# Optimization experiments

Measured on AMD Instinct MI355X. Metric: run time of the kernel, lower is better.

## Reference

```python
import jax, jax.numpy as jnp
import numpy as np

D_MODEL = 1024
EPS_DT = 1e-4
LN_EPS = 1e-5


def _layernorm(y, gamma, beta):
    mu = jnp.mean(y, axis=-1, keepdims=True)
    var = jnp.var(y, axis=-1, keepdims=True)
    return (y - mu) * jax.lax.rsqrt(var + LN_EPS) * gamma + beta


def setup_inputs() -> dict:
    key = jax.random.key(0)
    ks = jax.random.split(key, 8)
    B, T, D = 8, 4096, D_MODEL
    s = 1.0 / np.sqrt(D)  # ~ torch Linear default init scale
    return {
        "x": jax.random.normal(ks[0], (B, T, D), jnp.float32),
        "delta_t": jax.random.uniform(ks[1], (B, T, D), jnp.float32),
        "log_decay": jnp.zeros((D,), jnp.float32),
        "W_in": jax.random.uniform(ks[2], (D, D), jnp.float32, -s, s),
        "b_in": jax.random.uniform(ks[3], (D,), jnp.float32, -s, s),
        "W_gate": jax.random.uniform(ks[4], (D, D), jnp.float32, -s, s),
        "b_gate": jax.random.uniform(ks[5], (D,), jnp.float32, -s, s),
        "W_out": jax.random.uniform(ks[6], (D, D), jnp.float32, -s, s),
        "b_out": jax.random.uniform(ks[7], (D,), jnp.float32, -s, s),
        "gamma": jnp.ones((D,), jnp.float32),
        "beta": jnp.zeros((D,), jnp.float32),
    }


def reference(x, delta_t, log_decay, W_in, b_in, W_gate, b_gate, W_out, b_out, gamma, beta):
    B, T, D = x.shape
    decay = jax.nn.softplus(log_decay) + 1e-4          # [D]
    dt = jnp.maximum(delta_t, EPS_DT)                   # [B,T,D]
    lamb = jnp.exp(-decay * dt)                         # [B,T,D]
    # Drive terms depend only on x -> precompute in parallel (big GEMMs).
    update = jnp.einsum('btd,ed->bte', x, W_in) + b_in
    gate = jax.nn.sigmoid(jnp.einsum('btd,ed->bte', x, W_gate) + b_gate)
    drive = (1.0 - lamb) * gate * update                # [B,T,D]

    def step(state, inputs):
        l_t, d_t = inputs
        state = l_t * state + d_t
        return state, state

    state0 = jnp.zeros((B, D), x.dtype)
    final_state, states = jax.lax.scan(
        step, state0,
        (jnp.swapaxes(lamb, 0, 1), jnp.swapaxes(drive, 0, 1)))
    states = jnp.swapaxes(states, 0, 1)                 # [B,T,D]
    # dropout is identity in eval mode
    y = states + jnp.einsum('btd,ed->bte', states, W_out) + b_out
    out = _layernorm(y, gamma, beta)
    return out, final_state
```

## Files before the change

### kernel.cpp

```cpp
#include <hip/hip_runtime.h>
#include <hip/hip_bf16.h>

#define D_MODEL 1024
#define BATCH 8
#define SEQ 4096
#define MROWS (BATCH*SEQ)
#define NC 64
#define CL 64

typedef __attribute__((ext_vector_type(4))) float f32x4;
typedef __attribute__((ext_vector_type(8))) short s16x8;

__device__ __forceinline__ unsigned short f2bf(float f){
  union { float f; unsigned int u; } v; v.f = f;
  return (unsigned short)((v.u + 0x7fffu + ((v.u >> 16) & 1u)) >> 16);
}
__device__ __forceinline__ float bf2f(unsigned int bits){
  union { unsigned int u; float f; } v; v.u = bits << 16; return v.f;
}

__device__ __forceinline__ void gload16(const void* g, void* l){
  __builtin_amdgcn_global_load_lds(
      (const __attribute__((address_space(1))) unsigned int*)g,
      (__attribute__((address_space(3))) unsigned int*)l, 16, 0, 0);
}

__global__ __launch_bounds__(256)
void prep_all_kernel(const float* __restrict__ x,
                     const float* __restrict__ Wi, const float* __restrict__ Wg,
                     const float* __restrict__ Wo, const float* __restrict__ ld,
                     unsigned short* __restrict__ xb,
                     unsigned short* __restrict__ Wugb,
                     unsigned short* __restrict__ Wob,
                     float* __restrict__ decay, int nx4){
  const int b = blockIdx.x;
  if (b < 8192){
    int i = b*256 + threadIdx.x;
    for (; i < nx4; i += 8192*256){
      float4 v = ((const float4*)x)[i];
      ushort4 o;
      o.x = f2bf(v.x); o.y = f2bf(v.y); o.z = f2bf(v.z); o.w = f2bf(v.w);
      ((ushort4*)xb)[i] = o;
    }
  } else {
    const int i = (b-8192)*256 + threadIdx.x;
    float4 a = ((const float4*)Wi)[i]; ushort4 o;
    o.x=f2bf(a.x); o.y=f2bf(a.y); o.z=f2bf(a.z); o.w=f2bf(a.w); ((ushort4*)Wugb)[i]=o;
    a = ((const float4*)Wg)[i];
    o.x=f2bf(a.x); o.y=f2bf(a.y); o.z=f2bf(a.z); o.w=f2bf(a.w); ((ushort4*)Wugb)[i + D_MODEL*D_MODEL/4]=o;
    a = ((const float4*)Wo)[i];
    o.x=f2bf(a.x); o.y=f2bf(a.y); o.z=f2bf(a.z); o.w=f2bf(a.w); ((ushort4*)Wob)[i]=o;
    if (i < D_MODEL){
      float v = ld[i];
      float sp = fmaxf(v, 0.f) + log1pf(expf(-fabsf(v)));
      decay[i] = sp + 1e-4f;
    }
  }
}

__global__ __launch_bounds__(256, 3)
void gemm_ug_kernel(const unsigned short* __restrict__ Aglob,
                    const unsigned short* __restrict__ Bglob,
                    const float* __restrict__ b_in,
                    const float* __restrict__ b_gate,
                    unsigned short* __restrict__ ub,
                    unsigned short* __restrict__ gb)
{
  __shared__ unsigned short sA[128*64];
  __shared__ unsigned short sB[128*64];
  const int tid  = threadIdx.x;
  const int lane = tid & 63;
  const int wave = tid >> 6;
  const int wr = wave >> 1, wc = wave & 1;
  const int bid  = blockIdx.x;
  const int idx  = bid >> 3;
  const int xcd  = bid & 7;
  const int bcol = (idx & 15) * 128;
  const int brow = (xcd*32 + (idx >> 4)) * 128;

  const f32x4 zero = {0.f,0.f,0.f,0.f};
  f32x4 acc[4][4];
  #pragma unroll
  for (int a=0;a<4;a++)
    #pragma unroll
    for (int b=0;b<4;b++) acc[a][b]=zero;

  for (int kt = 0; kt < D_MODEL/64; ++kt){
    __syncthreads();
    #pragma unroll
    for (int i=0;i<4;i++){
      const int ob = i*256 + wave*64;
      const int o  = ob + lane;
      const int r  = o >> 3;
      const int c  = ((o & 7) ^ (r & 7)) * 16;
      gload16((const char*)Aglob + (size_t)(brow + r)*(D_MODEL*2) + (size_t)kt*128 + c,
              (char*)sA + (size_t)ob*16);
      gload16((const char*)Bglob + (size_t)(bcol + r)*(D_MODEL*2) + (size_t)kt*128 + c,
              (char*)sB + (size_t)ob*16);
    }
    __syncthreads();
    #pragma unroll
    for (int ks=0; ks<2; ++ks){
      s16x8 af[4], bf[4];
      #pragma unroll
      for (int mi=0; mi<4; mi++){
        const int row = wr*64 + mi*16 + (lane & 15);
        const int chunk = (ks*4 + (lane>>4)) ^ (row & 7);
        af[mi] = *(const s16x8*)((const char*)sA + row*128 + chunk*16);
      }
      #pragma unroll
      for (int ni=0; ni<4; ni++){
        const int n = wc*64 + ni*16 + (lane & 15);
        const int chunk = (ks*4 + (lane>>4)) ^ (n & 7);
        bf[ni] = *(const s16x8*)((const char*)sB + n*128 + chunk*16);
      }
      #pragma unroll
      for (int mi=0; mi<4; mi++)
        #pragma unroll
        for (int ni=0; ni<4; ni++)
          acc[mi][ni] = __builtin_amdgcn_mfma_f32_16x16x32_bf16(af[mi], bf[ni], acc[mi][ni], 0,0,0);
    }
  }

  const int half = bcol >> 10;
  const float* bias = half ? b_gate : b_in;
  unsigned short* Co = half ? gb : ub;
  const int cb = bcol & 1023;
  #pragma unroll
  for (int ni=0; ni<4; ni++){
    const int col = cb + wc*64 + ni*16 + (lane & 15);
    const float vb = bias[col];
    #pragma unroll
    for (int mi=0; mi<4; mi++){
      #pragma unroll
      for (int q=0; q<4; q++){
        const int row = brow + wr*64 + mi*16 + ((lane>>4)*4) + q;
        Co[(size_t)row*D_MODEL + col] = f2bf(acc[mi][ni][q] + vb);
      }
    }
  }
}

__global__ __launch_bounds__(256)
void scan_passA(const unsigned short* __restrict__ ub,
                const unsigned short* __restrict__ gb,
                const float* __restrict__ delta,
                const float* __restrict__ decay,
                unsigned int* __restrict__ pack,
                float* __restrict__ cA, float* __restrict__ cB){
  const int d0 = (blockIdx.x*256 + threadIdx.x)*2;
  const int c = blockIdx.y, b = blockIdx.z;
  const float dc0 = decay[d0], dc1 = decay[d0+1];
  size_t base = ((size_t)b*SEQ + (size_t)c*CL)*D_MODEL + d0;
  float A0=1.f, A1=1.f, s0=0.f, s1=0.f;
  #pragma unroll 4
  for (int t=0;t<CL;t++){
    const size_t idx = base + (size_t)t*D_MODEL;
    const unsigned int uu = *(const unsigned int*)(ub + idx);
    const unsigned int gg = *(const unsigned int*)(gb + idx);
    const float2 dv = *(const float2*)(delta + idx);
    const float u0 = bf2f(uu & 0xffffu), u1 = bf2f(uu >> 16);
    const float z0 = bf2f(gg & 0xffffu), z1 = bf2f(gg >> 16);
    const float g0 = 1.f/(1.f + __expf(-z0));
    const float g1 = 1.f/(1.f + __expf(-z1));
    const float lam0 = __expf(-dc0 * fmaxf(dv.x, 1e-4f));
    const float lam1 = __expf(-dc1 * fmaxf(dv.y, 1e-4f));
    const float om0 = 1.f - lam0, om1 = 1.f - lam1;
    const float dr0 = om0 * g0 * u0;
    const float dr1 = om1 * g1 * u1;
    uint2 pw;
    pw.x = ((unsigned int)f2bf(dr0) << 16) | (unsigned int)f2bf(om0);
    pw.y = ((unsigned int)f2bf(dr1) << 16) | (unsigned int)f2bf(om1);
    *(uint2*)(pack + idx) = pw;
    A0 *= lam0; A1 *= lam1;
    s0 = fmaf(lam0, s0, dr0);
    s1 = fmaf(lam1, s1, dr1);
  }
  const size_t ci = ((size_t)b*NC + c)*D_MODEL + d0;
  *(float2*)(cA+ci) = make_float2(A0,A1);
  *(float2*)(cB+ci) = make_float2(s0,s1);
}

__global__ __launch_bounds__(256)
void scan_passB(const float* __restrict__ cA, const float* __restrict__ cB,
                float* __restrict__ cS, float* __restrict__ fstate){
  const int d0 = (blockIdx.x*256 + threadIdx.x)*2;
  const int b = blockIdx.y;
  float s0=0.f, s1=0.f;
  for (int c=0;c<NC;c++){
    const size_t ci = ((size_t)b*NC + c)*D_MODEL + d0;
    *(float2*)(cS+ci) = make_float2(s0,s1);
    float2 a  = *(const float2*)(cA+ci);
    float2 bb = *(const float2*)(cB+ci);
    s0 = fmaf(a.x, s0, bb.x);
    s1 = fmaf(a.y, s1, bb.y);
  }
  *(float2*)(fstate + (size_t)b*D_MODEL + d0) = make_float2(s0,s1);
}

__global__ __launch_bounds__(256)
void scan_passC(const unsigned int* __restrict__ pack, const float* __restrict__ cS,
                unsigned short* __restrict__ statesb){
  const int d0 = (blockIdx.x*256 + threadIdx.x)*2;
  const int c = blockIdx.y, b = blockIdx.z;
  float2 sv = *(const float2*)(cS + ((size_t)b*NC + c)*D_MODEL + d0);
  float s0 = sv.x, s1 = sv.y;
  size_t base = ((size_t)b*SEQ + (size_t)c*CL)*D_MODEL + d0;
  #pragma unroll 8
  for (int t=0;t<CL;t++){
    uint2 p = *(const uint2*)(pack + base + (size_t)t*D_MODEL);
    float om0 = bf2f(p.x & 0xffffu), dr0 = bf2f(p.x >> 16);
    float om1 = bf2f(p.y & 0xffffu), dr1 = bf2f(p.y >> 16);
    s0 = fmaf(-om0, s0, s0) + dr0;
    s1 = fmaf(-om1, s1, s1) + dr1;
    unsigned int w = ((unsigned int)f2bf(s1) << 16) | (unsigned int)f2bf(s0);
    *(unsigned int*)(statesb + base + (size_t)t*D_MODEL) = w;
  }
}

__global__ __launch_bounds__(256, 3)
void gemm_out_kernel(const unsigned short* __restrict__ Sb,
                     const unsigned short* __restrict__ Wob,
                     const float* __restrict__ b_out,
                     unsigned short* __restrict__ yb)
{
  __shared__ unsigned short sA[128*64];
  __shared__ unsigned short sB[128*64];
  const int tid  = threadIdx.x;
  const int lane = tid & 63;
  const int wave = tid >> 6;
  const int wr = wave >> 1, wc = wave & 1;
  const int bid = blockIdx.x;
  const int swz = ((bid & 7) << 8) | (bid >> 3);
  const int bcol = (swz & 7) * 128;
  const int brow = (swz >> 3) * 128;

  const f32x4 zero = {0.f,0.f,0.f,0.f};
  f32x4 acc[4][4];
  #pragma unroll
  for (int a=0;a<4;a++)
    #pragma unroll
    for (int b=0;b<4;b++) acc[a][b]=zero;

  const int kt_res = (bcol >> 6) + wc;

  for (int kt = 0; kt < D_MODEL/64; ++kt){
    __syncthreads();
    #pragma unroll
    for (int i=0;i<4;i++){
      const int ob = i*256 + wave*64;
      const int o  = ob + lane;
      const int r  = o >> 3;
      const int c  = ((o & 7) ^ (r & 7)) * 16;
      gload16((const char*)Sb  + (size_t)(brow + r)*(D_MODEL*2) + (size_t)kt*128 + c,
              (char*)sA + (size_t)ob*16);
      gload16((const char*)Wob + (size_t)(bcol + r)*(D_MODEL*2) + (size_t)kt*128 + c,
              (char*)sB + (size_t)ob*16);
    }
    __syncthreads();
    #pragma unroll
    for (int ks=0; ks<2; ++ks){
      s16x8 af[4], bf[4];
      #pragma unroll
      for (int mi=0; mi<4; mi++){
        const int row = wr*64 + mi*16 + (lane & 15);
        const int chunk = (ks*4 + (lane>>4)) ^ (row & 7);
        af[mi] = *(const s16x8*)((const char*)sA + row*128 + chunk*16);
      }
      #pragma unroll
      for (int ni=0; ni<4; ni++){
        const int n = wc*64 + ni*16 + (lane & 15);
        const int chunk = (ks*4 + (lane>>4)) ^ (n & 7);
        bf[ni] = *(const s16x8*)((const char*)sB + n*128 + chunk*16);
      }
      #pragma unroll
      for (int mi=0; mi<4; mi++)
        #pragma unroll
        for (int ni=0; ni<4; ni++)
          acc[mi][ni] = __builtin_amdgcn_mfma_f32_16x16x32_bf16(af[mi], bf[ni], acc[mi][ni], 0,0,0);
    }
    if (kt == kt_res){
      #pragma unroll
      for (int ni=0; ni<4; ni++){
        #pragma unroll
        for (int mi=0; mi<4; mi++){
          #pragma unroll
          for (int q=0; q<4; q++){
            const int rl = wr*64 + mi*16 + ((lane>>4)*4) + q;
            const int cl = ni*16 + (lane & 15);
            const int byte = rl*128 + (((cl>>3) ^ (rl&7))*16) + ((cl&7)*2);
            acc[mi][ni][q] += bf2f((unsigned int)*(const unsigned short*)((const char*)sA + byte));
          }
        }
      }
    }
  }

  #pragma unroll
  for (int ni=0; ni<4; ni++){
    const int col = bcol + wc*64 + ni*16 + (lane & 15);
    const float vb = b_out[col];
    #pragma unroll
    for (int mi=0; mi<4; mi++){
      #pragma unroll
      for (int q=0; q<4; q++){
        const int row = brow + wr*64 + mi*16 + ((lane>>4)*4) + q;
        yb[(size_t)row*D_MODEL + col] = f2bf(acc[mi][ni][q] + vb);
      }
    }
  }
}

__global__ __launch_bounds__(256)
void ln_kernel(const unsigned short* __restrict__ yb,
               const float* __restrict__ gamma, const float* __restrict__ beta,
               float* __restrict__ out)
{
  const int row = blockIdx.x;
  const int tid = threadIdx.x;
  ushort4 yv = ((const ushort4*)(yb + (size_t)row*D_MODEL))[tid];
  float4 v;
  v.x = bf2f(yv.x); v.y = bf2f(yv.y); v.z = bf2f(yv.z); v.w = bf2f(yv.w);
  float s = v.x+v.y+v.z+v.w;
  float q = v.x*v.x + v.y*v.y + v.z*v.z + v.w*v.w;
  #pragma unroll
  for (int off=32; off>0; off>>=1){ s += __shfl_xor(s, off); q += __shfl_xor(q, off); }
  __shared__ float rs[4], rq[4];
  const int wave = tid>>6, lane = tid&63;
  if (lane==0){ rs[wave]=s; rq[wave]=q; }
  __syncthreads();
  float ts = rs[0]+rs[1]+rs[2]+rs[3];
  float tq = rq[0]+rq[1]+rq[2]+rq[3];
  float mu  = ts * (1.f/D_MODEL);
  float var = tq * (1.f/D_MODEL) - mu*mu;
  float inv = rsqrtf(var + 1e-5f);
  float4 g = ((const float4*)gamma)[tid];
  float4 b = ((const float4*)beta)[tid];
  float4 o;
  o.x = (v.x-mu)*inv*g.x + b.x;
  o.y = (v.y-mu)*inv*g.y + b.y;
  o.z = (v.z-mu)*inv*g.z + b.z;
  o.w = (v.w-mu)*inv*g.w + b.w;
  ((float4*)(out + (size_t)row*D_MODEL))[tid] = o;
}

extern "C" void kernel_launch(void* const* d_in, const int* in_sizes, int n_in,
                              void* d_out, int out_size, void* d_ws, size_t ws_size,
                              hipStream_t stream) {
  const float* x         = (const float*)d_in[0];
  const float* delta     = (const float*)d_in[1];
  const float* log_decay = (const float*)d_in[2];
  const float* W_in      = (const float*)d_in[3];
  const float* b_in      = (const float*)d_in[4];
  const float* W_gate    = (const float*)d_in[5];
  const float* b_gate    = (const float*)d_in[6];
  const float* W_out     = (const float*)d_in[7];
  const float* b_out     = (const float*)d_in[8];
  const float* gamma     = (const float*)d_in[9];
  const float* beta      = (const float*)d_in[10];

  char* w = (char*)d_ws;
  unsigned short* xb   = (unsigned short*)(w);
  unsigned short* Wugb = (unsigned short*)(w + 67108864);
  unsigned short* Wob  = (unsigned short*)(w + 71303168);
  float*          decay= (float*)        (w + 73400320);
  float*          cA   = (float*)        (w + 73404416);
  float*          cB   = (float*)        (w + 75501568);
  float*          cS   = (float*)        (w + 77598720);
  unsigned int*   pack = (unsigned int*) (w + 79695872);
  unsigned short* ybuf = (unsigned short*)pack;
  unsigned short* statesb = xb;

  float* out    = (float*)d_out;
  float* fstate = out + (size_t)MROWS*D_MODEL;
  unsigned short* ub = (unsigned short*)d_out;
  unsigned short* gb = ub + (size_t)MROWS*D_MODEL;

  hipLaunchKernelGGL(prep_all_kernel, dim3(9216), dim3(256), 0, stream,
                     x, W_in, W_gate, W_out, log_decay, xb, Wugb, Wob, decay, MROWS*D_MODEL/4);
  hipLaunchKernelGGL(gemm_ug_kernel, dim3(4096), dim3(256), 0, stream,
                     xb, Wugb, b_in, b_gate, ub, gb);
  hipLaunchKernelGGL(scan_passA, dim3(2,NC,BATCH), dim3(256), 0, stream,
                     ub, gb, delta, decay, pack, cA, cB);
  hipLaunchKernelGGL(scan_passB, dim3(2,BATCH), dim3(256), 0, stream, cA, cB, cS, fstate);
  hipLaunchKernelGGL(scan_passC, dim3(2,NC,BATCH), dim3(256), 0, stream, pack, cS, statesb);
  hipLaunchKernelGGL(gemm_out_kernel, dim3(2048), dim3(256), 0, stream,
                     statesb, Wob, b_out, ybuf);
  hipLaunchKernelGGL(ln_kernel, dim3(MROWS), dim3(256), 0, stream, ybuf, gamma, beta, out);
}
```

Before: 422.6 us.

## Fuse gate/drive computation into dual-output GEMM epilogue, interleave W_in/W_gate rows

The W_in and W_gate bf16 weights are interleaved in 64-row groups so each GEMM tile computes matching update and gate columns together. The epilogue then applies the biases, sigmoid, decay exponent from delta, and the drive product, and writes the packed (drive, 1-lambda) word directly. This removes the bf16 update/gate intermediates and their reread in scan pass A, which now only reads the pack. The cost is a heavier GEMM epilogue with uncoalesced scalar delta reads and pack writes, and lambda in pass A is rebuilt from bf16 (1-lambda), which loses precision.

New measurement: 404.3 us. 1.05x faster.

```diff
diff --git a/kernel.cpp b/kernel.cpp
--- a/kernel.cpp
+++ b/kernel.cpp
@@ -44,10 +44,16 @@
     }
   } else {
     const int i = (b-8192)*256 + threadIdx.x;
+    const int row  = i >> 8;
+    const int col4 = i & 255;
+    const int g    = row >> 6;
+    const int r    = row & 63;
     float4 a = ((const float4*)Wi)[i]; ushort4 o;
-    o.x=f2bf(a.x); o.y=f2bf(a.y); o.z=f2bf(a.z); o.w=f2bf(a.w); ((ushort4*)Wugb)[i]=o;
+    o.x=f2bf(a.x); o.y=f2bf(a.y); o.z=f2bf(a.z); o.w=f2bf(a.w);
+    ((ushort4*)Wugb)[(g*128 + r)*256 + col4] = o;
     a = ((const float4*)Wg)[i];
-    o.x=f2bf(a.x); o.y=f2bf(a.y); o.z=f2bf(a.z); o.w=f2bf(a.w); ((ushort4*)Wugb)[i + D_MODEL*D_MODEL/4]=o;
+    o.x=f2bf(a.x); o.y=f2bf(a.y); o.z=f2bf(a.z); o.w=f2bf(a.w);
+    ((ushort4*)Wugb)[(g*128 + 64 + r)*256 + col4] = o;
     a = ((const float4*)Wo)[i];
     o.x=f2bf(a.x); o.y=f2bf(a.y); o.z=f2bf(a.z); o.w=f2bf(a.w); ((ushort4*)Wob)[i]=o;
     if (i < D_MODEL){
@@ -59,12 +65,13 @@
 }
 
 __global__ __launch_bounds__(256, 3)
-void gemm_ug_kernel(const unsigned short* __restrict__ Aglob,
-                    const unsigned short* __restrict__ Bglob,
-                    const float* __restrict__ b_in,
-                    const float* __restrict__ b_gate,
-                    unsigned short* __restrict__ ub,
-                    unsigned short* __restrict__ gb)
+void gemm_dual64_kernel(const unsigned short* __restrict__ Xb,
+                        const unsigned short* __restrict__ Wugb,
+                        const float* __restrict__ b_in,
+                        const float* __restrict__ b_gate,
+                        const float* __restrict__ decay,
+                        const float* __restrict__ delta,
+                        unsigned int* __restrict__ pack)
 {
   __shared__ unsigned short sA[128*64];
   __shared__ unsigned short sB[128*64];
@@ -75,15 +82,16 @@
   const int bid  = blockIdx.x;
   const int idx  = bid >> 3;
   const int xcd  = bid & 7;
-  const int bcol = (idx & 15) * 128;
+  const int ct   = idx & 15;
+  const int bcol = ct * 64;
   const int brow = (xcd*32 + (idx >> 4)) * 128;
 
   const f32x4 zero = {0.f,0.f,0.f,0.f};
-  f32x4 acc[4][4];
+  f32x4 accU[4][2], accG[4][2];
   #pragma unroll
   for (int a=0;a<4;a++)
     #pragma unroll
-    for (int b=0;b<4;b++) acc[a][b]=zero;
+    for (int b=0;b<2;b++){ accU[a][b]=zero; accG[a][b]=zero; }
 
   for (int kt = 0; kt < D_MODEL/64; ++kt){
     __syncthreads();
@@ -93,15 +101,15 @@
       const int o  = ob + lane;
       const int r  = o >> 3;
       const int c  = ((o & 7) ^ (r & 7)) * 16;
-      gload16((const char*)Aglob + (size_t)(brow + r)*(D_MODEL*2) + (size_t)kt*128 + c,
+      gload16((const char*)Xb   + (size_t)(brow + r)*(D_MODEL*2) + (size_t)kt*128 + c,
               (char*)sA + (size_t)ob*16);
-      gload16((const char*)Bglob + (size_t)(bcol + r)*(D_MODEL*2) + (size_t)kt*128 + c,
+      gload16((const char*)Wugb + (size_t)(ct*128 + r)*(D_MODEL*2) + (size_t)kt*128 + c,
               (char*)sB + (size_t)ob*16);
     }
     __syncthreads();
     #pragma unroll
     for (int ks=0; ks<2; ++ks){
-      s16x8 af[4], bf[4];
+      s16x8 af[4], bu[2], bg[2];
       #pragma unroll
       for (int mi=0; mi<4; mi++){
         const int row = wr*64 + mi*16 + (lane & 15);
@@ -109,72 +117,60 @@
         af[mi] = *(const s16x8*)((const char*)sA + row*128 + chunk*16);
       }
       #pragma unroll
-      for (int ni=0; ni<4; ni++){
-        const int n = wc*64 + ni*16 + (lane & 15);
-        const int chunk = (ks*4 + (lane>>4)) ^ (n & 7);
-        bf[ni] = *(const s16x8*)((const char*)sB + n*128 + chunk*16);
+      for (int ni=0; ni<2; ni++){
+        const int nu = wc*32 + ni*16 + (lane & 15);
+        const int chunk = (ks*4 + (lane>>4)) ^ (nu & 7);
+        bu[ni] = *(const s16x8*)((const char*)sB + nu*128 + chunk*16);
+        bg[ni] = *(const s16x8*)((const char*)sB + (nu+64)*128 + chunk*16);
       }
       #pragma unroll
       for (int mi=0; mi<4; mi++)
         #pragma unroll
-        for (int ni=0; ni<4; ni++)
-          acc[mi][ni] = __builtin_amdgcn_mfma_f32_16x16x32_bf16(af[mi], bf[ni], acc[mi][ni], 0,0,0);
-    }
-  }
-
-  const int half = bcol >> 10;
-  const float* bias = half ? b_gate : b_in;
-  unsigned short* Co = half ? gb : ub;
-  const int cb = bcol & 1023;
-  #pragma unroll
-  for (int ni=0; ni<4; ni++){
-    const int col = cb + wc*64 + ni*16 + (lane & 15);
-    const float vb = bias[col];
+        for (int ni=0; ni<2; ni++){
+          accU[mi][ni] = __builtin_amdgcn_mfma_f32_16x16x32_bf16(af[mi], bu[ni], accU[mi][ni], 0,0,0);
+          accG[mi][ni] = __builtin_amdgcn_mfma_f32_16x16x32_bf16(af[mi], bg[ni], accG[mi][ni], 0,0,0);
+        }
+    }
+  }
+
+  #pragma unroll
+  for (int ni=0; ni<2; ni++){
+    const int col = bcol + wc*32 + ni*16 + (lane & 15);
+    const float vb = b_in[col], vg = b_gate[col], dc = decay[col];
     #pragma unroll
     for (int mi=0; mi<4; mi++){
       #pragma unroll
       for (int q=0; q<4; q++){
         const int row = brow + wr*64 + mi*16 + ((lane>>4)*4) + q;
-        Co[(size_t)row*D_MODEL + col] = f2bf(acc[mi][ni][q] + vb);
-      }
-    }
-  }
-}
-
-__global__ __launch_bounds__(256)
-void scan_passA(const unsigned short* __restrict__ ub,
-                const unsigned short* __restrict__ gb,
-                const float* __restrict__ delta,
-                const float* __restrict__ decay,
-                unsigned int* __restrict__ pack,
-                float* __restrict__ cA, float* __restrict__ cB){
+        const size_t idx2 = (size_t)row*D_MODEL + col;
+        const float u = accU[mi][ni][q] + vb;
+        const float z = accG[mi][ni][q] + vg;
+        const float g = 1.f/(1.f + __expf(-z));
+        const float dt = fmaxf(delta[idx2], 1e-4f);
+        const float lam = __expf(-dc*dt);
+        const float omla = 1.f - lam;
+        const float drv = omla * g * u;
+        pack[idx2] = ((unsigned int)f2bf(drv) << 16) | (unsigned int)f2bf(omla);
+      }
+    }
+  }
+}
+
+__global__ __launch_bounds__(256)
+void scan_passA(const unsigned int* __restrict__ pack, float* __restrict__ cA, float* __restrict__ cB){
   const int d0 = (blockIdx.x*256 + threadIdx.x)*2;
   const int c = blockIdx.y, b = blockIdx.z;
-  const float dc0 = decay[d0], dc1 = decay[d0+1];
   size_t base = ((size_t)b*SEQ + (size_t)c*CL)*D_MODEL + d0;
   float A0=1.f, A1=1.f, s0=0.f, s1=0.f;
-  #pragma unroll 4
+  #pragma unroll 8
   for (int t=0;t<CL;t++){
-    const size_t idx = base + (size_t)t*D_MODEL;
-    const unsigned int uu = *(const unsigned int*)(ub + idx);
-    const unsigned int gg = *(const unsigned int*)(gb + idx);
-    const float2 dv = *(const float2*)(delta + idx);
-    const float u0 = bf2f(uu & 0xffffu), u1 = bf2f(uu >> 16);
-    const float z0 = bf2f(gg & 0xffffu), z1 = bf2f(gg >> 16);
-    const float g0 = 1.f/(1.f + __expf(-z0));
-    const float g1 = 1.f/(1.f + __expf(-z1));
-    const float lam0 = __expf(-dc0 * fmaxf(dv.x, 1e-4f));
-    const float lam1 = __expf(-dc1 * fmaxf(dv.y, 1e-4f));
-    const float om0 = 1.f - lam0, om1 = 1.f - lam1;
-    const float dr0 = om0 * g0 * u0;
-    const float dr1 = om1 * g1 * u1;
-    uint2 pw;
-    pw.x = ((unsigned int)f2bf(dr0) << 16) | (unsigned int)f2bf(om0);
-    pw.y = ((unsigned int)f2bf(dr1) << 16) | (unsigned int)f2bf(om1);
-    *(uint2*)(pack + idx) = pw;
-    A0 *= lam0; A1 *= lam1;
-    s0 = fmaf(lam0, s0, dr0);
-    s1 = fmaf(lam1, s1, dr1);
+    uint2 p = *(const uint2*)(pack + base + (size_t)t*D_MODEL);
+    float om0 = bf2f(p.x & 0xffffu), dr0 = bf2f(p.x >> 16);
+    float om1 = bf2f(p.y & 0xffffu), dr1 = bf2f(p.y >> 16);
+    float l0 = 1.f - om0, l1 = 1.f - om1;
+    A0 *= l0; A1 *= l1;
+    s0 = fmaf(l0, s0, dr0);
+    s1 = fmaf(l1, s1, dr1);
   }
   const size_t ci = ((size_t)b*NC + c)*D_MODEL + d0;
   *(float2*)(cA+ci) = make_float2(A0,A1);
@@ -373,15 +369,12 @@
 
   float* out    = (float*)d_out;
   float* fstate = out + (size_t)MROWS*D_MODEL;
-  unsigned short* ub = (unsigned short*)d_out;
-  unsigned short* gb = ub + (size_t)MROWS*D_MODEL;
 
   hipLaunchKernelGGL(prep_all_kernel, dim3(9216), dim3(256), 0, stream,
                      x, W_in, W_gate, W_out, log_decay, xb, Wugb, Wob, decay, MROWS*D_MODEL/4);
-  hipLaunchKernelGGL(gemm_ug_kernel, dim3(4096), dim3(256), 0, stream,
-                     xb, Wugb, b_in, b_gate, ub, gb);
-  hipLaunchKernelGGL(scan_passA, dim3(2,NC,BATCH), dim3(256), 0, stream,
-                     ub, gb, delta, decay, pack, cA, cB);
+  hipLaunchKernelGGL(gemm_dual64_kernel, dim3(4096), dim3(256), 0, stream,
+                     xb, Wugb, b_in, b_gate, decay, delta, pack);
+  hipLaunchKernelGGL(scan_passA, dim3(2,NC,BATCH), dim3(256), 0, stream, pack, cA, cB);
   hipLaunchKernelGGL(scan_passB, dim3(2,BATCH), dim3(256), 0, stream, cA, cB, cS, fstate);
   hipLaunchKernelGGL(scan_passC, dim3(2,NC,BATCH), dim3(256), 0, stream, pack, cS, statesb);
   hipLaunchKernelGGL(gemm_out_kernel, dim3(2048), dim3(256), 0, stream,
```
